# Performance work log

Hardware: AMD Instinct MI355X
Metric: run time of the kernel (lower is better)

Reference implementation:

```python
import jax, jax.numpy as jnp
import numpy as np

B, H, S, D = 1, 16, 4096, 64

def setup_inputs() -> dict:
    key = jax.random.key(0)
    k1, k2, k3 = jax.random.split(key, 3)
    query = jax.random.normal(k1, (B, H, S, D), dtype=jnp.float32)
    key_t = jax.random.normal(k2, (B, H, S, D), dtype=jnp.float32)
    value = jax.random.normal(k3, (B, H, S, D), dtype=jnp.float32)
    attn_mask = jnp.zeros((B, 1, S, S), dtype=jnp.float32)
    return {"query": query, "key": key_t, "value": value, "attn_mask": attn_mask}

def reference(query, key, value, attn_mask):
    d = query.shape[-1]
    # [B,H,S,S] = QK^T / sqrt(d) + mask
    scores = jnp.einsum("bhqd,bhkd->bhqk", query, key) / jnp.sqrt(jnp.float32(d))
    scores = scores + attn_mask
    probs = jax.nn.softmax(scores, axis=-1)
    # dropout_p = 0.0 -> identity
    out = jnp.einsum("bhqk,bhkd->bhqd", probs, value)
    return out
```

## Files before the change

kernel.cpp:

```cpp
#include <hip/hip_runtime.h>
#include <stdint.h>

#define LOG2E  1.44269504088896f
#define QSCALE (0.125f * LOG2E)

typedef float    f32x4_t  __attribute__((ext_vector_type(4)));
typedef float    f32x16_t __attribute__((ext_vector_type(16)));
typedef _Float16 f16x8_t  __attribute__((ext_vector_type(8)));
typedef _Float16 f16x2_t  __attribute__((ext_vector_type(2)));

#if __has_builtin(__builtin_amdgcn_exp2f)
#define EXP2F(x) __builtin_amdgcn_exp2f(x)
#else
#define EXP2F(x) exp2f(x)
#endif

__device__ __forceinline__ float rowsum2(f16x2_t p, float acc) {
#if __has_builtin(__builtin_amdgcn_fdot2)
  return __builtin_amdgcn_fdot2(p, (f16x2_t){(_Float16)1.0f, (_Float16)1.0f}, acc, false);
#else
  return acc + (float)p[0] + (float)p[1];
#endif
}

__global__ void prep_kernel(const float* __restrict__ M, const float* __restrict__ K,
                            const float* __restrict__ V, _Float16* __restrict__ Kh,
                            _Float16* __restrict__ Vth, int* __restrict__ flag) {
  __shared__ __align__(16) _Float16 T[64 * 72];
  const int tid = threadIdx.x;
  const int bid = blockIdx.x;

  {
    const float* p = M + (size_t)bid * 8192 + (size_t)tid * 4;
    unsigned acc = 0;
#pragma unroll
    for (int i = 0; i < 8; ++i) {
      f32x4_t v = *(const f32x4_t*)(p + (size_t)i * 1024);
      acc |= __float_as_uint(v[0]) | __float_as_uint(v[1]) |
             __float_as_uint(v[2]) | __float_as_uint(v[3]);
    }
    if (acc & 0x7fffffffu) atomicOr(flag, 1);
  }

  if (Kh != nullptr) {
    {
      const size_t idx = ((size_t)bid * 256 + tid) * 8;
      f32x4_t a = *(const f32x4_t*)(K + idx);
      f32x4_t b = *(const f32x4_t*)(K + idx + 4);
      union { _Float16 h[8]; uint4 q; } U;
#pragma unroll
      for (int j = 0; j < 4; ++j) { U.h[j] = (_Float16)a[j]; U.h[4 + j] = (_Float16)b[j]; }
      *(uint4*)(Kh + idx) = U.q;
    }
    if (bid < 1024) {
      const int head = bid >> 6;
      const int st   = bid & 63;
      const size_t hoff = (size_t)head * 4096 * 64;
      const int sl    = tid >> 2;
      const int fbase = (tid & 3) * 16;
      const float* src = V + hoff + (size_t)(st * 64 + sl) * 64 + fbase;
#pragma unroll
      for (int c = 0; c < 4; ++c) {
        f32x4_t a = *(const f32x4_t*)(src + c * 4);
#pragma unroll
        for (int j = 0; j < 4; ++j) T[(fbase + c * 4 + j) * 72 + sl] = (_Float16)a[j];
      }
      __syncthreads();
      const int feat = tid >> 2;
      const int sb   = (tid & 3) * 16;
      uint4 r0 = *(const uint4*)&T[feat * 72 + sb];
      uint4 r1 = *(const uint4*)&T[feat * 72 + sb + 8];
      _Float16* dst = Vth + hoff + (size_t)feat * 4096 + st * 64 + sb;
      *(uint4*)(dst)     = r0;
      *(uint4*)(dst + 8) = r1;
    }
  }
}

template <bool WS16>
__launch_bounds__(256, 2)
__global__ void sdpa_kernel(const float* __restrict__ Qg, const float* __restrict__ Kg,
                            const float* __restrict__ Vg, const float* __restrict__ Mg,
                            const _Float16* __restrict__ Kh, const _Float16* __restrict__ Vth,
                            float* __restrict__ Og, const int* __restrict__ flag) {
  __shared__ __align__(16) _Float16 Ks[64 * 72];
  __shared__ __align__(16) _Float16 Vt[64 * 72];

  const int tid  = threadIdx.x;
  const int bid  = blockIdx.x;
  const int hh   = ((bid & 7) << 1) | ((bid >> 3) & 1);
  const int qt   = bid >> 4;
  const int w    = tid >> 6;
  const int lane = tid & 63;
  const int n    = lane & 31;
  const int h2   = lane >> 5;
  const int sig  = (n & 0x13) | ((n >> 1) & 4) | ((n << 1) & 8);
  const bool has_mask = (*flag) != 0;

  const size_t hoff = (size_t)hh * 4096 * 64;
  const int qcol = qt * 128 + w * 32 + n;

  f16x8_t qf[4];
  {
    const float* qp = Qg + hoff + (size_t)qcol * 64 + 8 * h2;
#pragma unroll
    for (int kh = 0; kh < 4; ++kh) {
      f32x4_t a = *(const f32x4_t*)(qp + kh * 16);
      f32x4_t b = *(const f32x4_t*)(qp + kh * 16 + 4);
      union { _Float16 h[8]; f16x8_t v; } U;
#pragma unroll
      for (int j = 0; j < 4; ++j) { U.h[j] = (_Float16)(a[j] * QSCALE); U.h[4 + j] = (_Float16)(b[j] * QSCALE); }
      qf[kh] = U.v;
    }
  }

  f32x16_t o0 = {0.f,0.f,0.f,0.f,0.f,0.f,0.f,0.f,0.f,0.f,0.f,0.f,0.f,0.f,0.f,0.f};
  f32x16_t o1 = o0;
  float lacc = 0.0f;

#pragma unroll 1
  for (int kt = 0; kt < 64; ++kt) {
    const int kbase = kt * 64;

    uint4 kk0, kk1, vv0, vv1;
    f32x4_t k0, k1, k2, k3;
    float vlo[8], vhi[8];
    if (WS16) {
      const _Float16* kp = Kh + hoff + (size_t)(kbase + (tid >> 2)) * 64 + (tid & 3) * 16;
      kk0 = *(const uint4*)(kp);
      kk1 = *(const uint4*)(kp + 8);
      const _Float16* vp = Vth + hoff + (size_t)(tid >> 2) * 4096 + kbase + (tid & 3) * 16;
      vv0 = *(const uint4*)(vp);
      vv1 = *(const uint4*)(vp + 8);
    } else {
      const float* kp = Kg + hoff + (size_t)(kbase + (tid >> 2)) * 64 + (tid & 3) * 16;
      k0 = *(const f32x4_t*)(kp + 0);
      k1 = *(const f32x4_t*)(kp + 4);
      k2 = *(const f32x4_t*)(kp + 8);
      k3 = *(const f32x4_t*)(kp + 12);
      const float* vp = Vg + hoff + (size_t)(kbase + (tid >> 5) * 8) * 64 + (tid & 31);
#pragma unroll
      for (int j = 0; j < 8; ++j) {
        vlo[j] = vp[(size_t)j * 64];
        vhi[j] = vp[(size_t)j * 64 + 32];
      }
    }

    f32x4_t mk[2][2][2];
    if (has_mask) {
      const float* mp = Mg + (size_t)qcol * 4096 + kbase + 8 * h2;
#pragma unroll
      for (int kb = 0; kb < 2; ++kb)
#pragma unroll
        for (int a = 0; a < 2; ++a)
#pragma unroll
          for (int b = 0; b < 2; ++b)
            mk[kb][a][b] = *(const f32x4_t*)(mp + kb * 32 + 16 * a + 4 * b);
    }

    __syncthreads();

    if (WS16) {
      *(uint4*)&Ks[(tid >> 2) * 72 + (tid & 3) * 16]     = kk0;
      *(uint4*)&Ks[(tid >> 2) * 72 + (tid & 3) * 16 + 8] = kk1;
      *(uint4*)&Vt[(tid >> 2) * 72 + (tid & 3) * 16]     = vv0;
      *(uint4*)&Vt[(tid >> 2) * 72 + (tid & 3) * 16 + 8] = vv1;
    } else {
      union { _Float16 h[8]; uint4 q; } A, B;
#pragma unroll
      for (int j = 0; j < 4; ++j) {
        A.h[j] = (_Float16)k0[j];  A.h[4 + j] = (_Float16)k1[j];
        B.h[j] = (_Float16)k2[j];  B.h[4 + j] = (_Float16)k3[j];
      }
      *(uint4*)&Ks[(tid >> 2) * 72 + (tid & 3) * 16]     = A.q;
      *(uint4*)&Ks[(tid >> 2) * 72 + (tid & 3) * 16 + 8] = B.q;
      union { _Float16 h[8]; uint4 q; } C, D;
#pragma unroll
      for (int j = 0; j < 8; ++j) { C.h[j] = (_Float16)vlo[j]; D.h[j] = (_Float16)vhi[j]; }
      *(uint4*)&Vt[(tid & 31) * 72 + (tid >> 5) * 8]        = C.q;
      *(uint4*)&Vt[((tid & 31) + 32) * 72 + (tid >> 5) * 8] = D.q;
    }

    __syncthreads();

#pragma unroll
    for (int kb = 0; kb < 2; ++kb) {
      f32x16_t acc = {0.f,0.f,0.f,0.f,0.f,0.f,0.f,0.f,0.f,0.f,0.f,0.f,0.f,0.f,0.f,0.f};
#pragma unroll
      for (int kh = 0; kh < 4; ++kh) {
        const f16x8_t ka = *(const f16x8_t*)&Ks[(kb * 32 + sig) * 72 + kh * 16 + 8 * h2];
        acc = __builtin_amdgcn_mfma_f32_32x32x16_f16(ka, qf[kh], acc, 0, 0, 0);
      }
#pragma unroll
      for (int a = 0; a < 2; ++a) {
        union { _Float16 h[8]; f16x8_t v; f16x2_t p2[4]; } F;
#pragma unroll
        for (int idx = 0; idx < 8; ++idx) {
          float x = acc[8 * a + idx];
          if (has_mask) x = __builtin_fmaf(mk[kb][a][idx >> 2][idx & 3], LOG2E, x);
          F.h[idx] = (_Float16)EXP2F(x);
        }
#pragma unroll
        for (int t = 0; t < 4; ++t) lacc = rowsum2(F.p2[t], lacc);
        const int f = kb * 2 + a;
        const f16x8_t v0 = *(const f16x8_t*)&Vt[n * 72 + f * 16 + 8 * h2];
        o0 = __builtin_amdgcn_mfma_f32_32x32x16_f16(F.v, v0, o0, 0, 0, 0);
        const f16x8_t v1 = *(const f16x8_t*)&Vt[(32 + n) * 72 + f * 16 + 8 * h2];
        o1 = __builtin_amdgcn_mfma_f32_32x32x16_f16(F.v, v1, o1, 0, 0, 0);
      }
    }
  }

  float lq = lacc + __shfl_xor(lacc, 32);
  float* op = Og + hoff;
#pragma unroll
  for (int r2 = 0; r2 < 4; ++r2) {
#pragma unroll
    for (int rr = 0; rr < 4; ++rr) {
      const int reg  = r2 * 4 + rr;
      const int qrow = rr + 8 * r2 + 4 * h2;
      float lr  = __shfl(lq, qrow);
      float inv = 1.0f / lr;
      const size_t row = (size_t)(qt * 128 + w * 32 + qrow) * 64;
      op[row + n]      = o0[reg] * inv;
      op[row + 32 + n] = o1[reg] * inv;
    }
  }
}

extern "C" void kernel_launch(void* const* d_in, const int* in_sizes, int n_in,
                              void* d_out, int out_size, void* d_ws, size_t ws_size,
                              hipStream_t stream) {
  const float* Q = (const float*)d_in[0];
  const float* K = (const float*)d_in[1];
  const float* V = (const float*)d_in[2];
  const float* M = (const float*)d_in[3];
  float* O = (float*)d_out;

  const size_t NELEM  = (size_t)16 * 4096 * 64;
  const size_t need16 = 256 + 2 * NELEM * sizeof(_Float16);
  int* flag = (int*)d_ws;
  const bool ws16 = (ws_size >= need16);
  _Float16* Kh  = ws16 ? (_Float16*)((char*)d_ws + 256) : nullptr;
  _Float16* Vth = ws16 ? Kh + NELEM : nullptr;

  hipMemsetAsync(flag, 0, sizeof(int), stream);
  prep_kernel<<<2048, 256, 0, stream>>>(M, K, V, Kh, Vth, flag);

  if (ws16) {
    sdpa_kernel<true><<<512, 256, 0, stream>>>(Q, K, V, M, Kh, Vth, O, flag);
  } else {
    sdpa_kernel<false><<<512, 256, 0, stream>>>(Q, K, V, M, nullptr, nullptr, O, flag);
  }
}
```

Baseline: 232.3 us.

## Split key range across two half-blocks and merge partial outputs in LDS

Adds a 512-thread kernel in which each half of the block processes half of the key tiles for the same 128-query tile, with separate LDS buffers per half. The partial output accumulators and row sums are then combined through shared memory before normalisation and the store. The aim is to double the waves per block to improve latency hiding and cut the serial key loop length. The cost is more LDS, a reduction step at the end, and higher register pressure under the tighter launch bounds. It relies on no running max being tracked, so partial sums can simply be added.

Result: faster. 227.0 us, median of 2 (-2.3%).

```diff
diff --git a/kernel.cpp b/kernel.cpp
--- a/kernel.cpp
+++ b/kernel.cpp
@@ -77,12 +77,155 @@
   }
 }
 
-template <bool WS16>
+__launch_bounds__(512, 2)
+__global__ void sdpa_split(const float* __restrict__ Qg, const float* __restrict__ Mg,
+                           const _Float16* __restrict__ Kh, const _Float16* __restrict__ Vth,
+                           float* __restrict__ Og, const int* __restrict__ flag) {
+  __shared__ __align__(16) _Float16 Ks[2][64 * 72];
+  __shared__ __align__(16) _Float16 Vt[2][64 * 72];
+
+  const int tid   = threadIdx.x;
+  const int bid   = blockIdx.x;
+  const int khalf = tid >> 8;
+  const int ht    = tid & 255;
+  const int hh    = ((bid & 7) << 1) | ((bid >> 3) & 1);
+  const int qt    = bid >> 4;
+  const int w     = ht >> 6;
+  const int lane  = tid & 63;
+  const int n     = lane & 31;
+  const int h2    = lane >> 5;
+  const int sig   = (n & 0x13) | ((n >> 1) & 4) | ((n << 1) & 8);
+  const bool has_mask = (*flag) != 0;
+
+  const size_t hoff = (size_t)hh * 4096 * 64;
+  const int qcol = qt * 128 + w * 32 + n;
+  const int ktlo = khalf * 32;
+
+  f16x8_t qf[4];
+  {
+    const float* qp = Qg + hoff + (size_t)qcol * 64 + 8 * h2;
+#pragma unroll
+    for (int kh = 0; kh < 4; ++kh) {
+      f32x4_t a = *(const f32x4_t*)(qp + kh * 16);
+      f32x4_t b = *(const f32x4_t*)(qp + kh * 16 + 4);
+      union { _Float16 h[8]; f16x8_t v; } U;
+#pragma unroll
+      for (int j = 0; j < 4; ++j) { U.h[j] = (_Float16)(a[j] * QSCALE); U.h[4 + j] = (_Float16)(b[j] * QSCALE); }
+      qf[kh] = U.v;
+    }
+  }
+
+  f32x16_t o0 = {0.f,0.f,0.f,0.f,0.f,0.f,0.f,0.f,0.f,0.f,0.f,0.f,0.f,0.f,0.f,0.f};
+  f32x16_t o1 = o0;
+  float lacc = 0.0f;
+
+#pragma unroll 1
+  for (int kk = 0; kk < 32; ++kk) {
+    const int kbase = (ktlo + kk) * 64;
+
+    uint4 kk0, kk1, vv0, vv1;
+    {
+      const _Float16* kp = Kh + hoff + (size_t)(kbase + (ht >> 2)) * 64 + (ht & 3) * 16;
+      kk0 = *(const uint4*)(kp);
+      kk1 = *(const uint4*)(kp + 8);
+      const _Float16* vp = Vth + hoff + (size_t)(ht >> 2) * 4096 + kbase + (ht & 3) * 16;
+      vv0 = *(const uint4*)(vp);
+      vv1 = *(const uint4*)(vp + 8);
+    }
+
+    f32x4_t mk[2][2][2];
+    if (has_mask) {
+      const float* mp = Mg + (size_t)qcol * 4096 + kbase + 8 * h2;
+#pragma unroll
+      for (int kb = 0; kb < 2; ++kb)
+#pragma unroll
+        for (int a = 0; a < 2; ++a)
+#pragma unroll
+          for (int b = 0; b < 2; ++b)
+            mk[kb][a][b] = *(const f32x4_t*)(mp + kb * 32 + 16 * a + 4 * b);
+    }
+
+    __syncthreads();
+
+    *(uint4*)&Ks[khalf][(ht >> 2) * 72 + (ht & 3) * 16]     = kk0;
+    *(uint4*)&Ks[khalf][(ht >> 2) * 72 + (ht & 3) * 16 + 8] = kk1;
+    *(uint4*)&Vt[khalf][(ht >> 2) * 72 + (ht & 3) * 16]     = vv0;
+    *(uint4*)&Vt[khalf][(ht >> 2) * 72 + (ht & 3) * 16 + 8] = vv1;
+
+    __syncthreads();
+
+#pragma unroll
+    for (int kb = 0; kb < 2; ++kb) {
+      f32x16_t acc = {0.f,0.f,0.f,0.f,0.f,0.f,0.f,0.f,0.f,0.f,0.f,0.f,0.f,0.f,0.f,0.f};
+#pragma unroll
+      for (int kh = 0; kh < 4; ++kh) {
+        const f16x8_t ka = *(const f16x8_t*)&Ks[khalf][(kb * 32 + sig) * 72 + kh * 16 + 8 * h2];
+        acc = __builtin_amdgcn_mfma_f32_32x32x16_f16(ka, qf[kh], acc, 0, 0, 0);
+      }
+#pragma unroll
+      for (int a = 0; a < 2; ++a) {
+        union { _Float16 h[8]; f16x8_t v; f16x2_t p2[4]; } F;
+#pragma unroll
+        for (int idx = 0; idx < 8; ++idx) {
+          float x = acc[8 * a + idx];
+          if (has_mask) x = __builtin_fmaf(mk[kb][a][idx >> 2][idx & 3], LOG2E, x);
+          F.h[idx] = (_Float16)EXP2F(x);
+        }
+#pragma unroll
+        for (int t = 0; t < 4; ++t) lacc = rowsum2(F.p2[t], lacc);
+        const int f = kb * 2 + a;
+        const f16x8_t v0 = *(const f16x8_t*)&Vt[khalf][n * 72 + f * 16 + 8 * h2];
+        o0 = __builtin_amdgcn_mfma_f32_32x32x16_f16(F.v, v0, o0, 0, 0, 0);
+        const f16x8_t v1 = *(const f16x8_t*)&Vt[khalf][(32 + n) * 72 + f * 16 + 8 * h2];
+        o1 = __builtin_amdgcn_mfma_f32_32x32x16_f16(F.v, v1, o1, 0, 0, 0);
+      }
+    }
+  }
+
+  float* const Xo0 = (float*)&Ks[0][0];
+  float* const Xo1 = (float*)&Vt[0][0];
+  float* const Xl  = Xo0 + 4096;
+
+  __syncthreads();
+  if (khalf == 1) {
+#pragma unroll
+    for (int reg = 0; reg < 16; ++reg) {
+      Xo0[(w * 16 + reg) * 64 + lane] = o0[reg];
+      Xo1[(w * 16 + reg) * 64 + lane] = o1[reg];
+    }
+    Xl[w * 64 + lane] = lacc;
+  }
+  __syncthreads();
+  if (khalf == 0) {
+#pragma unroll
+    for (int reg = 0; reg < 16; ++reg) {
+      o0[reg] += Xo0[(w * 16 + reg) * 64 + lane];
+      o1[reg] += Xo1[(w * 16 + reg) * 64 + lane];
+    }
+    lacc += Xl[w * 64 + lane];
+
+    float lq = lacc + __shfl_xor(lacc, 32);
+    float* op = Og + hoff;
+#pragma unroll
+    for (int r2 = 0; r2 < 4; ++r2) {
+#pragma unroll
+      for (int rr = 0; rr < 4; ++rr) {
+        const int reg  = r2 * 4 + rr;
+        const int qrow = rr + 8 * r2 + 4 * h2;
+        float lr  = __shfl(lq, qrow);
+        float inv = 1.0f / lr;
+        const size_t row = (size_t)(qt * 128 + w * 32 + qrow) * 64;
+        op[row + n]      = o0[reg] * inv;
+        op[row + 32 + n] = o1[reg] * inv;
+      }
+    }
+  }
+}
+
 __launch_bounds__(256, 2)
-__global__ void sdpa_kernel(const float* __restrict__ Qg, const float* __restrict__ Kg,
-                            const float* __restrict__ Vg, const float* __restrict__ Mg,
-                            const _Float16* __restrict__ Kh, const _Float16* __restrict__ Vth,
-                            float* __restrict__ Og, const int* __restrict__ flag) {
+__global__ void sdpa_fallback(const float* __restrict__ Qg, const float* __restrict__ Kg,
+                              const float* __restrict__ Vg, const float* __restrict__ Mg,
+                              float* __restrict__ Og, const int* __restrict__ flag) {
   __shared__ __align__(16) _Float16 Ks[64 * 72];
   __shared__ __align__(16) _Float16 Vt[64 * 72];
 
@@ -121,18 +264,9 @@
 #pragma unroll 1
   for (int kt = 0; kt < 64; ++kt) {
     const int kbase = kt * 64;
-
-    uint4 kk0, kk1, vv0, vv1;
     f32x4_t k0, k1, k2, k3;
     float vlo[8], vhi[8];
-    if (WS16) {
-      const _Float16* kp = Kh + hoff + (size_t)(kbase + (tid >> 2)) * 64 + (tid & 3) * 16;
-      kk0 = *(const uint4*)(kp);
-      kk1 = *(const uint4*)(kp + 8);
-      const _Float16* vp = Vth + hoff + (size_t)(tid >> 2) * 4096 + kbase + (tid & 3) * 16;
-      vv0 = *(const uint4*)(vp);
-      vv1 = *(const uint4*)(vp + 8);
-    } else {
+    {
       const float* kp = Kg + hoff + (size_t)(kbase + (tid >> 2)) * 64 + (tid & 3) * 16;
       k0 = *(const f32x4_t*)(kp + 0);
       k1 = *(const f32x4_t*)(kp + 4);
@@ -145,7 +279,6 @@
         vhi[j] = vp[(size_t)j * 64 + 32];
       }
     }
-
     f32x4_t mk[2][2][2];
     if (has_mask) {
       const float* mp = Mg + (size_t)qcol * 4096 + kbase + 8 * h2;
@@ -159,13 +292,7 @@
     }
 
     __syncthreads();
-
-    if (WS16) {
-      *(uint4*)&Ks[(tid >> 2) * 72 + (tid & 3) * 16]     = kk0;
-      *(uint4*)&Ks[(tid >> 2) * 72 + (tid & 3) * 16 + 8] = kk1;
-      *(uint4*)&Vt[(tid >> 2) * 72 + (tid & 3) * 16]     = vv0;
-      *(uint4*)&Vt[(tid >> 2) * 72 + (tid & 3) * 16 + 8] = vv1;
-    } else {
+    {
       union { _Float16 h[8]; uint4 q; } A, B;
 #pragma unroll
       for (int j = 0; j < 4; ++j) {
@@ -180,7 +307,6 @@
       *(uint4*)&Vt[(tid & 31) * 72 + (tid >> 5) * 8]        = C.q;
       *(uint4*)&Vt[((tid & 31) + 32) * 72 + (tid >> 5) * 8] = D.q;
     }
-
     __syncthreads();
 
 #pragma unroll
@@ -248,8 +374,8 @@
   prep_kernel<<<2048, 256, 0, stream>>>(M, K, V, Kh, Vth, flag);
 
   if (ws16) {
-    sdpa_kernel<true><<<512, 256, 0, stream>>>(Q, K, V, M, Kh, Vth, O, flag);
+    sdpa_split<<<512, 512, 0, stream>>>(Q, M, Kh, Vth, O, flag);
   } else {
-    sdpa_kernel<false><<<512, 256, 0, stream>>>(Q, K, V, M, nullptr, nullptr, O, flag);
-  }
-}
+    sdpa_fallback<<<512, 256, 0, stream>>>(Q, K, V, M, O, flag);
+  }
+}
```
